# Performance work log

Hardware: AMD Instinct MI355X
Metric: run time of the kernel (lower is better)

Reference implementation:

```python
import jax, jax.numpy as jnp
import numpy as np

B, T, E, H = 8, 2048, 1024, 128


def setup_inputs() -> dict:
    key = jax.random.key(0)
    kx, kk, kq, kv = jax.random.split(key, 4)
    x = jax.random.normal(kx, (B, T, E), dtype=jnp.float32)
    # nn.Linear(E, H, bias=False) weights, stored as (E, H) so y = x @ W
    scale = 0.02
    Wk = jax.random.normal(kk, (E, H), dtype=jnp.float32) * scale
    Wq = jax.random.normal(kq, (E, H), dtype=jnp.float32) * scale
    Wv = jax.random.normal(kv, (E, H), dtype=jnp.float32) * scale
    return {"x": x, "Wk": Wk, "Wq": Wq, "Wv": Wv}


def reference(x, Wk, Wq, Wv):
    # x: (B,T,E) -> k,q,v: (B,T,H)
    k = x @ Wk
    q = x @ Wq
    v = x @ Wv
    # att[b,t,s] = q[b,t] . k[b,s]
    att = jnp.einsum('bth,bsh->bts', q, k)
    # original: att / head_norm, head_norm = 1/sqrt(H)  => multiply by sqrt(H)
    att = att * jnp.sqrt(jnp.float32(H))
    tril = jnp.tril(jnp.ones((T, T), dtype=bool))
    att = jnp.where(tril, att, -jnp.inf)
    # original softmax over dim=1 (query axis), NOT the key axis
    att = jax.nn.softmax(att, axis=1)
    return att @ v  # (B,T,H)
```

## Files before the change

### kernel.cpp

```cpp
#include <hip/hip_runtime.h>
#include <math.h>

#define Bn 8
#define Tn 2048
#define En 1024
#define Hn 128
#define SQRTH 11.313708498984761f

typedef __attribute__((ext_vector_type(8))) short short8;
typedef __attribute__((ext_vector_type(8))) _Float16 half8;
typedef __attribute__((ext_vector_type(4))) short short4v;
typedef __attribute__((ext_vector_type(4))) float float4v;

#define MFMA16(a, b, c)  __builtin_amdgcn_mfma_f32_16x16x32_bf16((a), (b), (c), 0, 0, 0)
#define MFMA16F(a, b, c) __builtin_amdgcn_mfma_f32_16x16x32_f16((a), (b), (c), 0, 0, 0)

static __device__ __forceinline__ unsigned short f2bf(float f) {
    unsigned u = __float_as_uint(f);
    u += 0x7FFFu + ((u >> 16) & 1u);
    return (unsigned short)(u >> 16);
}
static __device__ __forceinline__ unsigned short f2h(float f) {
    _Float16 h = (_Float16)f;
    union { _Float16 v; unsigned short u; } c; c.v = h; return c.u;
}

static __device__ __forceinline__ void gll16(const unsigned short* g, unsigned short* l) {
    __builtin_amdgcn_global_load_lds(
        (const __attribute__((address_space(1))) unsigned int*)g,
        (__attribute__((address_space(3))) unsigned int*)l, 16, 0, 0);
}


__global__ __launch_bounds__(256) void wtrans_kernel(
    const float* __restrict__ Wq, const float* __restrict__ Wk, const float* __restrict__ Wv,
    unsigned short* __restrict__ wtt)
{
    int t = blockIdx.x * 256 + threadIdx.x;
    int kc8 = t & 3;
    int hh = (t >> 2) & 127;
    int ks = (t >> 9) & 31;
    int z = t >> 14;
    const float* W = (z == 0) ? Wq : ((z == 1) ? Wk : Wv);
    short8 h8;
#pragma unroll
    for (int j = 0; j < 8; j++) {
        int e = ks * 32 + kc8 * 8 + j;
        h8[j] = (short)f2h(W[(size_t)e * Hn + hh]);
    }
    size_t d = (((size_t)z * 32 + ks) * 4096) + (size_t)hh * 32
             + (size_t)(kc8 ^ (hh & 3)) * 8;
    *(short8*)(wtt + d) = h8;
}

__global__ __launch_bounds__(256) void xconv_kernel(
    const float* __restrict__ x, unsigned short* __restrict__ xt)
{
    int g = blockIdx.x * 256 + threadIdx.x;
    int kc8 = g & 3;
    int rr = (g >> 2) & 63;
    int ks = (g >> 8) & 31;
    int mt = g >> 13;
    size_t src = ((size_t)mt * 64 + rr) * En + ks * 32 + kc8 * 8;
    float4v f0 = *(const float4v*)(x + src);
    float4v f1 = *(const float4v*)(x + src + 4);
    short8 h;
#pragma unroll
    for (int j = 0; j < 4; j++) {
        h[j] = (short)f2h(f0[j]);
        h[j + 4] = (short)f2h(f1[j]);
    }
    size_t d = (size_t)(g >> 2) * 32 + (size_t)(kc8 ^ (rr & 3)) * 8;
    *(short8*)(xt + d) = h;
}

__global__ __launch_bounds__(256) void proj_kernel(
    const unsigned short* __restrict__ xt, const unsigned short* __restrict__ wtt,
    unsigned short* __restrict__ qf, unsigned short* __restrict__ kf,
    unsigned short* __restrict__ vtt)
{
    __shared__ __align__(16) unsigned short lds[2][6144];
    int z = blockIdx.y;
    int mt = blockIdx.x;
    int tid = threadIdx.x;
    int wave = tid >> 6, lane = tid & 63;
    int c15 = lane & 15, kg = lane >> 4;
    int sb = c15 & 3;
    int mrow = wave >> 1, ncol = wave & 1;

    const unsigned short* A0 = xt + (size_t)mt * 32 * 2048;
    const unsigned short* B0 = wtt + (size_t)z * 32 * 4096;

    float4v acc[2][4];
#pragma unroll
    for (int i = 0; i < 2; i++)
#pragma unroll
        for (int j = 0; j < 4; j++) acc[i][j] = (float4v)0.0f;

    const unsigned short* gcur[3];
    int lbo[3];
    int gstep[3];
#pragma unroll
    for (int i = 0; i < 3; i++) {
        int ch = wave * 3 + i;
        if (ch < 4) { gcur[i] = A0 + ch * 512;       lbo[i] = ch * 512;        gstep[i] = 2048; }
        else        { gcur[i] = B0 + (ch - 4) * 512; lbo[i] = 2048 + (ch - 4) * 512; gstep[i] = 4096; }
    }
    int lo8 = lane * 8;

    auto stage = [&](int buf) {
        unsigned short* Lb = lds[0] + buf * 6144;
#pragma unroll
        for (int i = 0; i < 3; i++) {
            gll16(gcur[i] + lo8, Lb + lbo[i] + lo8);
            gcur[i] += gstep[i];
        }
    };

    stage(0);

    for (int ks = 0; ks < 32; ks++) {
        __syncthreads();
        if (ks + 1 < 32) stage((ks + 1) & 1);
        const unsigned short* Lb = lds[ks & 1];

        half8 ah[2], bh[4];
#pragma unroll
        for (int mi = 0; mi < 2; mi++) {
            int row = mrow * 32 + mi * 16 + c15;
            ah[mi] = *(const half8*)(Lb + row * 32 + (kg ^ sb) * 8);
        }
#pragma unroll
        for (int ni = 0; ni < 4; ni++) {
            int row = ncol * 64 + ni * 16 + c15;
            bh[ni] = *(const half8*)(Lb + 2048 + row * 32 + (kg ^ sb) * 8);
        }
#pragma unroll
        for (int mi = 0; mi < 2; mi++)
#pragma unroll
            for (int ni = 0; ni < 4; ni++)
                acc[mi][ni] = MFMA16F(ah[mi], bh[ni], acc[mi][ni]);
    }

    if (z < 2) {
        unsigned short* oh = (z == 0) ? qf : kf;
#pragma unroll
        for (int mi = 0; mi < 2; mi++) {
#pragma unroll
            for (int ni = 0; ni < 4; ni++) {
                int h = ncol * 64 + ni * 16 + c15;
#pragma unroll
                for (int r = 0; r < 4; r++) {
                    int t = mt * 64 + mrow * 32 + mi * 16 + kg * 4 + r;
                    size_t o = (size_t)t * Hn + (((h >> 3) ^ (t & 15)) << 3) + (h & 7);
                    oh[o] = f2h(acc[mi][ni][r]);
                }
            }
        }
    } else {
        int b = mt >> 5;
#pragma unroll
        for (int mi = 0; mi < 2; mi++) {
            int t0 = (mt & 31) * 64 + mrow * 32 + mi * 16 + kg * 4;
            int sc = t0 >> 5, so = t0 & 31;
#pragma unroll
            for (int ni = 0; ni < 4; ni++) {
                int h = ncol * 64 + ni * 16 + c15;
                short4v pk;
#pragma unroll
                for (int r = 0; r < 4; r++) pk[r] = (short)f2bf(acc[mi][ni][r]);
                int so2 = ((((so >> 3) ^ ((h >> 1) & 3))) << 3) | (so & 7);
                *(short4v*)(vtt + (((size_t)b * 64 + sc) * 128 + h) * 32 + so2) = pk;
            }
        }
    }
}

__global__ __launch_bounds__(256) void stats_part_kernel(
    const unsigned short* __restrict__ qf, const unsigned short* __restrict__ kf,
    float* __restrict__ m_part, float* __restrict__ l_part)
{
    __shared__ __align__(16) unsigned short lds[4096];
    int tid = threadIdx.x;
    int wave = tid >> 6, lane = tid & 63;
    int c15 = lane & 15, kg = lane >> 4;
    int b = blockIdx.x;

    int rem = (int)blockIdx.y, sj, nch = 1;
    for (sj = 0; sj < 32; sj++) {
        nch = ((31 - sj) >> 2) + 1;
        if (rem < nch) break;
        rem -= nch;
    }
    int ci = rem;
    int c0 = 2 * sj;
    int len = 64 - c0;
    int cbase = len / nch, ext = len % nch;
    int cs = c0 + ci * cbase + (ci < ext ? ci : ext);
    int ce = cs + cbase + (ci < ext ? 1 : 0);

    int s_base = sj * 64 + wave * 16;

    half8 a[4];
    {
        int s = s_base + c15;
        const unsigned short* kr = kf + ((size_t)(b * Tn + s)) * Hn;
#pragma unroll
        for (int st = 0; st < 4; st++) {
            int off = ((st * 4 + kg) ^ c15) * 8;
            a[st] = *(const half8*)(kr + off);
        }
    }
    float m[4], l[4];
#pragma unroll
    for (int r = 0; r < 4; r++) { m[r] = -3.0e38f; l[r] = 0.0f; }

    auto stage = [&](int c) {
        const unsigned short* Qf = qf + ((size_t)b * Tn + c * 32) * Hn;
        int lo8 = lane * 8;
#pragma unroll
        for (int i = 0; i < 2; i++) {
            int ch = wave * 2 + i;
            gll16(Qf + ch * 512 + lo8, lds + ch * 512 + lo8);
        }
    };

    for (int c = cs; c < ce; c++) {
        stage(c);
        __syncthreads();
#pragma unroll
        for (int half = 0; half < 2; half++) {
            int t16 = c * 32 + half * 16;
            int tl = half * 16 + c15;
            float4v a1 = (float4v)0.0f;
#pragma unroll
            for (int st = 0; st < 4; st++) {
                int off = tl * 128 + ((st * 4 + kg) ^ c15) * 8;
                half8 bh = *(const half8*)(lds + off);
                a1 = MFMA16F(a[st], bh, a1);
            }
            int t = t16 + c15;
#pragma unroll
            for (int r = 0; r < 4; r++) {
                float attv = a1[r] * SQRTH;
                int s_row = s_base + kg * 4 + r;
                bool valid = (t >= s_row);
                float cand = valid ? attv : -3.0e38f;
                float mn = fmaxf(m[r], cand);
                l[r] = l[r] * __expf(m[r] - mn) + (valid ? __expf(attv - mn) : 0.0f);
                m[r] = mn;
            }
        }
        __syncthreads();
    }
#pragma unroll
    for (int mask = 1; mask < 16; mask <<= 1) {
#pragma unroll
        for (int r = 0; r < 4; r++) {
            float mo = __shfl_xor(m[r], mask);
            float lo2 = __shfl_xor(l[r], mask);
            float mn = fmaxf(m[r], mo);
            l[r] = l[r] * __expf(m[r] - mn) + lo2 * __expf(mo - mn);
            m[r] = mn;
        }
    }
    if (c15 == 0) {
#pragma unroll
        for (int r = 0; r < 4; r++) {
            int sl = wave * 16 + kg * 4 + r;
            size_t d = ((((size_t)b * 32 + sj) * 8 + ci) * 64) + sl;
            m_part[d] = m[r];
            l_part[d] = l[r];
        }
    }
}

__global__ __launch_bounds__(256) void stats_combine_kernel(
    const float* __restrict__ m_part, const float* __restrict__ l_part,
    float* __restrict__ m_st, float* __restrict__ il_st)
{
    int g = blockIdx.x * 256 + threadIdx.x;
    int s = g & 2047, b = g >> 11;
    int sj = s >> 6, sl = s & 63;
    int nch = ((31 - sj) >> 2) + 1;
    size_t base = (((size_t)b * 32 + sj) * 8) * 64 + sl;
    float M = m_part[base];
    float L = l_part[base];
    for (int ci = 1; ci < nch; ci++) {
        float mi = m_part[base + (size_t)ci * 64];
        float li = l_part[base + (size_t)ci * 64];
        float mn = fmaxf(M, mi);
        L = L * __expf(M - mn) + li * __expf(mi - mn);
        M = mn;
    }
    m_st[(size_t)b * Tn + s] = M;
    il_st[(size_t)b * Tn + s] = 1.0f / L;
}

__global__ __launch_bounds__(256) void out_part_kernel(
    const unsigned short* __restrict__ qf, const unsigned short* __restrict__ kf,
    const unsigned short* __restrict__ vtt,
    const float* __restrict__ m_st, const float* __restrict__ il_st,
    float* __restrict__ part_out)
{
    __shared__ __align__(16) unsigned short lds[8192];
    __shared__ __align__(16) unsigned short pbuf[4][16][40];
    int tid = threadIdx.x;
    int wave = tid >> 6, lane = tid & 63;
    int c15 = lane & 15, kg = lane >> 4;
    int b = blockIdx.x;

    int rem = (int)blockIdx.y, tj, nch = 1;
    for (tj = 31; tj >= 0; tj--) {
        nch = (tj >> 2) + 1;
        if (rem < nch) break;
        rem -= nch;
    }
    int ci = rem;
    int len = 2 * tj + 2;
    int cbase = len / nch, ext = len % nch;
    int cs = ci * cbase + (ci < ext ? ci : ext);
    int ce = cs + cbase + (ci < ext ? 1 : 0);

    int t_base = tj * 64 + wave * 16;

    half8 qa[4];
    {
        int t = t_base + c15;
        const unsigned short* qr = qf + ((size_t)(b * Tn + t)) * Hn;
#pragma unroll
        for (int st = 0; st < 4; st++) {
            int off = ((st * 4 + kg) ^ c15) * 8;
            qa[st] = *(const half8*)(qr + off);
        }
    }
    float4v oacc[8];
#pragma unroll
    for (int i = 0; i < 8; i++) oacc[i] = (float4v)0.0f;

    auto stage = [&](int c) {
        const unsigned short* Kf = kf + ((size_t)b * Tn + c * 32) * Hn;
        const unsigned short* Vv = vtt + ((size_t)b * 64 + c) * (128 * 32);
        int lo8 = lane * 8;
#pragma unroll
        for (int i = 0; i < 4; i++) {
            int ch = wave * 4 + i;
            const unsigned short* g;
            unsigned short* ld;
            if (ch < 8) { g = Kf + ch * 512;       ld = lds + ch * 512; }
            else        { g = Vv + (ch - 8) * 512; ld = lds + 4096 + (ch - 8) * 512; }
            gll16(g + lo8, ld + lo8);
        }
    };

    for (int c = cs; c < ce; c++) {
        stage(c);
        __syncthreads();
#pragma unroll
        for (int half = 0; half < 2; half++) {
            int s16 = c * 32 + half * 16;
            int sl = half * 16 + c15;
            float4v a1 = (float4v)0.0f;
#pragma unroll
            for (int st = 0; st < 4; st++) {
                int off = sl * 128 + ((st * 4 + kg) ^ c15) * 8;
                half8 bh = *(const half8*)(lds + off);
                a1 = MFMA16F(qa[st], bh, a1);
            }
            float msv = m_st[b * Tn + s16 + c15];
            float ilv = il_st[b * Tn + s16 + c15];
#pragma unroll
            for (int r = 0; r < 4; r++) {
                int t = t_base + kg * 4 + r;
                float attv = a1[r] * SQRTH;
                float earg = fminf(attv - msv, 0.0f);
                float p = (t >= s16 + c15) ? __expf(earg) * ilv : 0.0f;
                pbuf[wave][kg * 4 + r][c15 + half * 16] = f2bf(p);
            }
        }
        short8 pa = *(const short8*)&pbuf[wave][c15][kg * 8];
#pragma unroll
        for (int nt = 0; nt < 8; nt++) {
            int voff = (nt * 16 + c15) * 32 + ((kg ^ ((c15 >> 1) & 3)) * 8);
            short8 vb = *(const short8*)(lds + 4096 + voff);
            oacc[nt] = MFMA16(pa, vb, oacc[nt]);
        }
        __syncthreads();
    }
    float* po = part_out + ((((size_t)b * 32 + tj) * 8 + ci) * 64) * 128;
#pragma unroll
    for (int nt = 0; nt < 8; nt++) {
        int h = nt * 16 + c15;
#pragma unroll
        for (int r = 0; r < 4; r++) {
            int tl = wave * 16 + kg * 4 + r;
            po[(size_t)tl * 128 + h] = oacc[nt][r];
        }
    }
}

__global__ __launch_bounds__(256) void out_combine_kernel(
    const float* __restrict__ part_out, float* __restrict__ out)
{
    int g = blockIdx.x * 256 + threadIdx.x;
    int h4 = g & 31;
    int t = (g >> 5) & 2047;
    int b = g >> 16;
    int tj = t >> 6, tl = t & 63;
    int nch = (tj >> 2) + 1;
    const float4v* p = (const float4v*)(part_out
        + ((((size_t)b * 32 + tj) * 8) * 64 + tl) * 128) + h4;
    float4v acc = p[0];
    for (int ci = 1; ci < nch; ci++) acc += p[(size_t)ci * 2048];
    *((float4v*)(out + ((size_t)b * Tn + t) * Hn) + h4) = acc;
}

extern "C" void kernel_launch(void* const* d_in, const int* in_sizes, int n_in,
                              void* d_out, int out_size, void* d_ws, size_t ws_size,
                              hipStream_t stream)
{
    (void)in_sizes; (void)n_in; (void)out_size; (void)ws_size;
    const float* x  = (const float*)d_in[0];
    const float* Wk = (const float*)d_in[1];
    const float* Wq = (const float*)d_in[2];
    const float* Wv = (const float*)d_in[3];
    float* out = (float*)d_out;

    const size_t NQ = (size_t)Bn * Tn * Hn;
    const size_t NX = (size_t)Bn * Tn * En;
    unsigned short* qf  = (unsigned short*)d_ws;
    unsigned short* qlo = qf + NQ;
    unsigned short* kf  = qlo + NQ;
    unsigned short* klo = kf + NQ;
    unsigned short* vtt  = klo + NQ;
    unsigned short* xt   = vtt + NQ;
    unsigned short* xt_lo = xt + NX;
    unsigned short* wtt  = xt_lo + NX;
    unsigned short* wtt_lo = wtt + (size_t)3 * Hn * En;
    float* m_st  = (float*)(wtt_lo + (size_t)3 * Hn * En);
    float* il_st = m_st + (size_t)Bn * Tn;

    float* part_out = (float*)xt;
    float* m_part   = (float*)wtt;
    float* l_part   = (float*)wtt_lo;

    wtrans_kernel<<<dim3(192), 256, 0, stream>>>(Wq, Wk, Wv, wtt);
    xconv_kernel<<<dim3(8192), 256, 0, stream>>>(x, xt);
    proj_kernel<<<dim3(256, 3), 256, 0, stream>>>(xt, wtt, qf, kf, vtt);
    stats_part_kernel<<<dim3(Bn, 144), 256, 0, stream>>>(qf, kf, m_part, l_part);
    stats_combine_kernel<<<dim3(64), 256, 0, stream>>>(m_part, l_part, m_st, il_st);
    out_part_kernel<<<dim3(Bn, 144), 256, 0, stream>>>(qf, kf, vtt,
                                                       m_st, il_st, part_out);
    out_combine_kernel<<<dim3(2048), 256, 0, stream>>>(part_out, out);
}
```

Before: 178.3 us.

## Double-buffer LDS staging in stats and output attention kernels

Both the stats and output kernels now use two LDS buffers. The next chunk's global-to-LDS load is issued right after the barrier, while the current chunk is being computed, and the trailing barrier in each loop iteration is removed. The goal is to hide global load latency behind MFMA work and to halve the barriers per chunk. In exchange, LDS use per block doubles, which may lower occupancy, and the loop now relies on the single top-of-loop barrier also waiting for the outstanding async loads.

```diff
diff --git a/kernel.cpp b/kernel.cpp
--- a/kernel.cpp
+++ b/kernel.cpp
@@ -180,7 +180,7 @@
     const unsigned short* __restrict__ qf, const unsigned short* __restrict__ kf,
     float* __restrict__ m_part, float* __restrict__ l_part)
 {
-    __shared__ __align__(16) unsigned short lds[4096];
+    __shared__ __align__(16) unsigned short lds[2][4096];
     int tid = threadIdx.x;
     int wave = tid >> 6, lane = tid & 63;
     int c15 = lane & 15, kg = lane >> 4;
@@ -215,19 +215,33 @@
 #pragma unroll
     for (int r = 0; r < 4; r++) { m[r] = -3.0e38f; l[r] = 0.0f; }
 
-    auto stage = [&](int c) {
-        const unsigned short* Qf = qf + ((size_t)b * Tn + c * 32) * Hn;
-        int lo8 = lane * 8;
+    const unsigned short* gcur[2];
+    int lbo[2];
+    {
+        const unsigned short* Qf = qf + ((size_t)b * Tn + cs * 32) * Hn;
 #pragma unroll
         for (int i = 0; i < 2; i++) {
             int ch = wave * 2 + i;
-            gll16(Qf + ch * 512 + lo8, lds + ch * 512 + lo8);
+            gcur[i] = Qf + ch * 512;
+            lbo[i] = ch * 512;
+        }
+    }
+    int lo8 = lane * 8;
+
+    auto stage = [&](int buf) {
+        unsigned short* Lb = lds[0] + buf * 4096;
+#pragma unroll
+        for (int i = 0; i < 2; i++) {
+            gll16(gcur[i] + lo8, Lb + lbo[i] + lo8);
+            gcur[i] += 4096;
         }
     };
 
+    stage(0);
     for (int c = cs; c < ce; c++) {
-        stage(c);
         __syncthreads();
+        if (c + 1 < ce) stage((c - cs + 1) & 1);
+        const unsigned short* Lb = lds[0] + ((c - cs) & 1) * 4096;
 #pragma unroll
         for (int half = 0; half < 2; half++) {
             int t16 = c * 32 + half * 16;
@@ -236,7 +250,7 @@
 #pragma unroll
             for (int st = 0; st < 4; st++) {
                 int off = tl * 128 + ((st * 4 + kg) ^ c15) * 8;
-                half8 bh = *(const half8*)(lds + off);
+                half8 bh = *(const half8*)(Lb + off);
                 a1 = MFMA16F(a[st], bh, a1);
             }
             int t = t16 + c15;
@@ -251,7 +265,6 @@
                 m[r] = mn;
             }
         }
-        __syncthreads();
     }
 #pragma unroll
     for (int mask = 1; mask < 16; mask <<= 1) {
@@ -303,7 +316,7 @@
     const float* __restrict__ m_st, const float* __restrict__ il_st,
     float* __restrict__ part_out)
 {
-    __shared__ __align__(16) unsigned short lds[8192];
+    __shared__ __align__(16) unsigned short lds[2][8192];
     __shared__ __align__(16) unsigned short pbuf[4][16][40];
     int tid = threadIdx.x;
     int wave = tid >> 6, lane = tid & 63;
@@ -338,24 +351,34 @@
 #pragma unroll
     for (int i = 0; i < 8; i++) oacc[i] = (float4v)0.0f;
 
-    auto stage = [&](int c) {
-        const unsigned short* Kf = kf + ((size_t)b * Tn + c * 32) * Hn;
-        const unsigned short* Vv = vtt + ((size_t)b * 64 + c) * (128 * 32);
-        int lo8 = lane * 8;
+    const unsigned short* gcur[4];
+    int lbo[4];
+    {
+        const unsigned short* Kf = kf + ((size_t)b * Tn + cs * 32) * Hn;
+        const unsigned short* Vv = vtt + ((size_t)b * 64 + cs) * (128 * 32);
 #pragma unroll
         for (int i = 0; i < 4; i++) {
             int ch = wave * 4 + i;
-            const unsigned short* g;
-            unsigned short* ld;
-            if (ch < 8) { g = Kf + ch * 512;       ld = lds + ch * 512; }
-            else        { g = Vv + (ch - 8) * 512; ld = lds + 4096 + (ch - 8) * 512; }
-            gll16(g + lo8, ld + lo8);
+            if (ch < 8) { gcur[i] = Kf + ch * 512;       lbo[i] = ch * 512; }
+            else        { gcur[i] = Vv + (ch - 8) * 512; lbo[i] = 4096 + (ch - 8) * 512; }
+        }
+    }
+    int lo8 = lane * 8;
+
+    auto stage = [&](int buf) {
+        unsigned short* Lb = lds[0] + buf * 8192;
+#pragma unroll
+        for (int i = 0; i < 4; i++) {
+            gll16(gcur[i] + lo8, Lb + lbo[i] + lo8);
+            gcur[i] += 4096;
         }
     };
 
+    stage(0);
     for (int c = cs; c < ce; c++) {
-        stage(c);
         __syncthreads();
+        if (c + 1 < ce) stage((c - cs + 1) & 1);
+        const unsigned short* Lb = lds[0] + ((c - cs) & 1) * 8192;
 #pragma unroll
         for (int half = 0; half < 2; half++) {
             int s16 = c * 32 + half * 16;
@@ -364,7 +387,7 @@
 #pragma unroll
             for (int st = 0; st < 4; st++) {
                 int off = sl * 128 + ((st * 4 + kg) ^ c15) * 8;
-                half8 bh = *(const half8*)(lds + off);
+                half8 bh = *(const half8*)(Lb + off);
                 a1 = MFMA16F(qa[st], bh, a1);
             }
             float msv = m_st[b * Tn + s16 + c15];
@@ -382,10 +405,9 @@
 #pragma unroll
         for (int nt = 0; nt < 8; nt++) {
             int voff = (nt * 16 + c15) * 32 + ((kg ^ ((c15 >> 1) & 3)) * 8);
-            short8 vb = *(const short8*)(lds + 4096 + voff);
+            short8 vb = *(const short8*)(Lb + 4096 + voff);
             oacc[nt] = MFMA16(pa, vb, oacc[nt]);
         }
-        __syncthreads();
     }
     float* po = part_out + ((((size_t)b * 32 + tj) * 8 + ci) * 64) * 128;
 #pragma unroll
```

Measured after the change: 180.8 us. No clear change (+1.4%).
